# Kernel optimization log

Hardware: AMD Instinct MI355X
Metric: run time of the kernel (lower is better)

## Reference

```python
import jax, jax.numpy as jnp
import numpy as np

N_NODES = 50000
N_RAND_EDGES = 1_600_000
IN_FEATS = 512
HIDDEN = 256
NUM_CLASSES = 64


def setup_inputs() -> dict:
    key = jax.random.key(0)
    ks = jax.random.split(key, 6)
    src = jax.random.randint(ks[0], (N_RAND_EDGES,), 0, N_NODES, dtype=jnp.int32)
    dst = jax.random.randint(ks[1], (N_RAND_EDGES,), 0, N_NODES, dtype=jnp.int32)
    # dgl.add_self_loop(g): append (i, i) for every node
    loop = jnp.arange(N_NODES, dtype=jnp.int32)
    src = jnp.concatenate([src, loop])
    dst = jnp.concatenate([dst, loop])
    features = jax.random.normal(ks[2], (N_NODES, IN_FEATS), dtype=jnp.float32)
    W_conv = jax.random.normal(ks[3], (IN_FEATS, HIDDEN), dtype=jnp.float32) * (1.0 / np.sqrt(IN_FEATS))
    b_conv = jnp.zeros((HIDDEN,), dtype=jnp.float32)
    W2 = jax.random.normal(ks[4], (HIDDEN, NUM_CLASSES), dtype=jnp.float32) * (1.0 / np.sqrt(HIDDEN))
    b2 = jnp.zeros((NUM_CLASSES,), dtype=jnp.float32)
    return {"features": features, "W_conv": W_conv, "b_conv": b_conv,
            "W2": W2, "b2": b2, "src": src, "dst": dst}


def reference(features, W_conv, b_conv, W2, b2, src, dst):
    N = features.shape[0]
    ones = jnp.ones(src.shape[0], dtype=features.dtype)
    # symmetric ('both') normalization as in DGL GraphConv; self-loops guarantee deg >= 1
    deg_out = jax.ops.segment_sum(ones, src, num_segments=N)
    deg_in = jax.ops.segment_sum(ones, dst, num_segments=N)
    norm_src = jax.lax.rsqrt(deg_out)[:, None]  # [N, 1]
    norm_dst = jax.lax.rsqrt(deg_in)[:, None]
    # in_feats > hidden -> DGL multiplies by the weight before aggregating
    h = (features @ W_conv) * norm_src            # [N, H]
    agg = jax.ops.segment_sum(h[src], dst, num_segments=N)  # sparse SpMM: gather + scatter-add
    x = jax.nn.relu(agg * norm_dst + b_conv)      # [N, H]
    # dropout: identity in eval mode (deterministic reference)
    logits = x @ W2 + b2                          # [N, C]
    return jax.nn.log_softmax(logits, axis=1)
```

## Files before the change

kernel.cpp:

```cpp
#include <hip/hip_runtime.h>

typedef unsigned char u8;
typedef unsigned short u16;
typedef unsigned int u32;
typedef __attribute__((ext_vector_type(4))) float f32x4;
typedef __attribute__((ext_vector_type(8))) short s16x8;
typedef __attribute__((ext_vector_type(4))) unsigned short u16x4;
typedef __attribute__((ext_vector_type(8))) unsigned short u16x8;

#define IN_FEATS 512
#define HIDDEN   256
#define NCLS     64
#define NB       256
#define HBINS    25000
#define EPT      7

#define H8_CLIP  2.5f
#define H8_INV   (127.0f / H8_CLIP)
#define H8_SCALE (H8_CLIP / 127.0f)

static __device__ inline u16 f2bf(float f) {
    unsigned int u = __builtin_bit_cast(unsigned int, f);
    unsigned int r = (u + 0x7FFFu + ((u >> 16) & 1u)) >> 16;
    return (u16)r;
}


__launch_bounds__(1024)
__global__ void khist(const int* __restrict__ src, const int* __restrict__ dst,
                      u16* __restrict__ P,
                      const float* __restrict__ W, u16* __restrict__ Wt,
                      const float* __restrict__ W2, u16* __restrict__ W2t,
                      signed char* __restrict__ h8, int E, int N) {
    __shared__ u32 pk[25000];
    const int b = blockIdx.x;
    const int t = threadIdx.x;
    const int lo = (int)((long)b * E / NB);
    const int hi = (int)((long)(b + 1) * E / NB);

    {
        int g = b * 1024 + t;
        if (g < IN_FEATS * HIDDEN) {
            int k = g >> 8, n = g & 255;
            Wt[n * IN_FEATS + k] = f2bf(W[g]);
        } else if (g < IN_FEATS * HIDDEN + HIDDEN * NCLS) {
            int ii = g - IN_FEATS * HIDDEN;
            int k = ii >> 6, n = ii & 63;
            W2t[n * HIDDEN + k] = f2bf(W2[ii]);
        } else if (g < IN_FEATS * HIDDEN + HIDDEN * NCLS + 64) {
            ((int*)(h8 + (size_t)N * HIDDEN))[g - IN_FEATS * HIDDEN - HIDDEN * NCLS] = 0;
        }
    }

    int se[EPT], de[EPT];
#pragma unroll
    for (int p = 0; p < EPT; p++) {
        int e = lo + t + p * 1024;
        se[p] = 0; de[p] = 0;
        if (e < hi) { se[p] = src[e]; de[p] = dst[e]; }
    }

#pragma unroll 1
    for (int half = 0; half < 2; half++) {
        const int base = half * HBINS;
        __syncthreads();
        for (int j = t; j < 25000; j += 1024) pk[j] = 0;
        __syncthreads();
#pragma unroll
        for (int p = 0; p < EPT; p++) {
            int e = lo + t + p * 1024;
            if (e < hi) {
                unsigned rs = (unsigned)(se[p] - base), rd = (unsigned)(de[p] - base);
                if (rs < (unsigned)HBINS) atomicAdd(&pk[rs >> 1], 1u << ((rs & 1) << 4));
                if (rd < (unsigned)HBINS) atomicAdd(&pk[12500 + (rd >> 1)], 1u << ((rd & 1) << 4));
            }
        }
        for (int e = lo + t + EPT * 1024; e < hi; e += 1024) {
            int s = src[e], d = dst[e];
            unsigned rs = (unsigned)(s - base), rd = (unsigned)(d - base);
            if (rs < (unsigned)HBINS) atomicAdd(&pk[rs >> 1], 1u << ((rs & 1) << 4));
            if (rd < (unsigned)HBINS) atomicAdd(&pk[12500 + (rd >> 1)], 1u << ((rd & 1) << 4));
        }
        __syncthreads();
        for (int j = t; j < HBINS; j += 1024) {
            u32 o  = (pk[j >> 1] >> ((j & 1) << 4)) & 0xffffu;
            u32 in = (pk[12500 + (j >> 1)] >> ((j & 1) << 4)) & 0xffffu;
            P[(size_t)b * 50000 + base + j] = (u16)((o & 0xffu) | ((in & 0xffu) << 8));
        }
    }
}

__launch_bounds__(256)
__global__ void kredscan(u16* __restrict__ P, int* __restrict__ rowptr,
                         int* __restrict__ bsum, float* __restrict__ ns,
                         float* __restrict__ nd, int N) {
    __shared__ int wsum[4];
    const int b = blockIdx.x, t = threadIdx.x;
    const int lane = t & 63, wave = t >> 6;
    const int j = b * 256 + t;
    u32 si = 0;
    if (j < N) {
        u32 so = 0;
#pragma unroll 8
        for (int bb = 0; bb < NB; bb++) {
            u32 v = P[(size_t)bb * 50000 + j];
            P[(size_t)bb * 50000 + j] = (u16)si;
            so += v & 0xffu;
            si += v >> 8;
        }
        ns[j] = rsqrtf((float)so);
        nd[j] = rsqrtf((float)si);
    }
    int v = (j < N) ? (int)si : 0;
    int s = v;
#pragma unroll
    for (int off = 1; off < 64; off <<= 1) {
        int u = __shfl_up(s, off);
        if (lane >= off) s += u;
    }
    if (lane == 63) wsum[wave] = s;
    __syncthreads();
    int woff = 0;
#pragma unroll
    for (int w = 0; w < 4; w++) woff += (w < wave) ? wsum[w] : 0;
    if (j < N) rowptr[j] = woff + s - v;
    if (t == 255) bsum[b] = woff + s;
}

__launch_bounds__(256)
__global__ void kscanB(int* __restrict__ rowptr, const int* __restrict__ bsum,
                       int N, int nblk, int E) {
    __shared__ int wsum[4];
    const int b = blockIdx.x, t = threadIdx.x;
    const int lane = t & 63, wave = t >> 6;
    int v = (t < b && t < nblk) ? bsum[t] : 0;
#pragma unroll
    for (int off = 32; off; off >>= 1) v += __shfl_xor(v, off);
    if (lane == 0) wsum[wave] = v;
    __syncthreads();
    int offsum = wsum[0] + wsum[1] + wsum[2] + wsum[3];
    int j = b * 256 + t;
    if (j < N) rowptr[j] += offsum;
    if (b == 0 && t == 0) rowptr[N] = E;
}

__launch_bounds__(1024)
__global__ void kscat(const int* __restrict__ src, const int* __restrict__ dst,
                      const int* __restrict__ rowptr, const u16* __restrict__ P,
                      int* __restrict__ csc, int E, int N) {
    __shared__ int cur[HBINS];
    const int b = blockIdx.x;
    const int t = threadIdx.x;
    const int lo = (int)((long)b * E / NB);
    const int hi = (int)((long)(b + 1) * E / NB);

    int se[EPT], de[EPT];
#pragma unroll
    for (int p = 0; p < EPT; p++) {
        int e = lo + t + p * 1024;
        se[p] = 0; de[p] = 0;
        if (e < hi) { se[p] = src[e]; de[p] = dst[e]; }
    }

#pragma unroll 1
    for (int half = 0; half < 2; half++) {
        const int base = half * HBINS;
        __syncthreads();
        for (int j = t; j < HBINS; j += 1024) {
            int node = base + j;
            cur[j] = (node < N) ? rowptr[node] + (int)P[(size_t)b * 50000 + node] : 0;
        }
        __syncthreads();
#pragma unroll
        for (int p = 0; p < EPT; p++) {
            int e = lo + t + p * 1024;
            if (e < hi) {
                unsigned rd = (unsigned)(de[p] - base);
                if (rd < (unsigned)HBINS) {
                    int pos = atomicAdd(&cur[rd], 1);
                    csc[pos] = se[p] << 8;
                }
            }
        }
        for (int e = lo + t + EPT * 1024; e < hi; e += 1024) {
            int d = dst[e];
            unsigned rd = (unsigned)(d - base);
            if (rd < (unsigned)HBINS) {
                int pos = atomicAdd(&cur[rd], 1);
                csc[pos] = src[e] << 8;
            }
        }
    }
}


static __device__ inline s16x8 ld_frag(const u16* p) {
    u16x4 lo = *(const u16x4*)p;
    u16x4 hi = *(const u16x4*)(p + 4);
    s16x8 r;
    r[0] = (short)lo.x; r[1] = (short)lo.y; r[2] = (short)lo.z; r[3] = (short)lo.w;
    r[4] = (short)hi.x; r[5] = (short)hi.y; r[6] = (short)hi.z; r[7] = (short)hi.w;
    return r;
}

__launch_bounds__(512)
__global__ void k_gemm1(const float* __restrict__ feat, const u16* __restrict__ Wt,
                        const float* __restrict__ norm_src, signed char* __restrict__ h8, int N) {
    __shared__ __align__(16) u16 At[128][40];
    __shared__ __align__(16) u16 Bt[256][40];
    const int t = threadIdx.x;
    const int lane = t & 63;
    const int wave = t >> 6;
    const int wm = wave & 1;
    const int wn = wave >> 1;
    const int m0 = blockIdx.x * 128;
    const int l15 = lane & 15;
    const int l4 = lane >> 4;

    const int r0a = t >> 3, qa = t & 7;
    const int r1a = (t + 512) >> 3;
    const int gr0 = m0 + r0a, gr1 = m0 + r1a;

    float4 pa0, pa1;
    auto LOADA = [&](int kk) {
        pa0 = (gr0 < N) ? *(const float4*)&feat[(size_t)gr0 * IN_FEATS + kk + qa * 4]
                        : make_float4(0.f, 0.f, 0.f, 0.f);
        pa1 = (gr1 < N) ? *(const float4*)&feat[(size_t)gr1 * IN_FEATS + kk + qa * 4]
                        : make_float4(0.f, 0.f, 0.f, 0.f);
    };

    f32x4 acc[4][4] = {};
    LOADA(0);

    for (int kk = 0; kk < IN_FEATS; kk += 32) {
        __syncthreads();
        {
            u16x4 p;
            p.x = f2bf(pa0.x); p.y = f2bf(pa0.y); p.z = f2bf(pa0.z); p.w = f2bf(pa0.w);
            *(u16x4*)&At[r0a][qa * 4] = p;
            p.x = f2bf(pa1.x); p.y = f2bf(pa1.y); p.z = f2bf(pa1.z); p.w = f2bf(pa1.w);
            *(u16x4*)&At[r1a][qa * 4] = p;
        }
#pragma unroll
        for (int rnd = 0; rnd < 2; rnd++) {
            int slot = t + rnd * 512;
            int r = slot >> 2, q = slot & 3;
            u16x4 w0 = *(const u16x4*)&Wt[(size_t)r * IN_FEATS + kk + q * 8];
            u16x4 w1 = *(const u16x4*)&Wt[(size_t)r * IN_FEATS + kk + q * 8 + 4];
            *(u16x4*)&Bt[r][q * 8] = w0;
            *(u16x4*)&Bt[r][q * 8 + 4] = w1;
        }
        if (kk + 32 < IN_FEATS) LOADA(kk + 32);
        __syncthreads();

        s16x8 a[4], b[4];
#pragma unroll
        for (int mi = 0; mi < 4; mi++) a[mi] = ld_frag(&At[wm * 64 + mi * 16 + l15][l4 * 8]);
#pragma unroll
        for (int ni = 0; ni < 4; ni++) b[ni] = ld_frag(&Bt[wn * 64 + ni * 16 + l15][l4 * 8]);
#pragma unroll
        for (int mi = 0; mi < 4; mi++)
#pragma unroll
            for (int ni = 0; ni < 4; ni++)
                acc[mi][ni] = __builtin_amdgcn_mfma_f32_16x16x32_bf16(a[mi], b[ni], acc[mi][ni], 0, 0, 0);
    }

#pragma unroll
    for (int mi = 0; mi < 4; mi++) {
#pragma unroll
        for (int q = 0; q < 4; q++) {
            int row = m0 + wm * 64 + mi * 16 + l4 * 4 + q;
            if (row < N) {
                float nsv = norm_src[row] * H8_INV;
#pragma unroll
                for (int ni = 0; ni < 4; ni++) {
                    int col = wn * 64 + ni * 16 + l15;
                    int v = (int)rintf(acc[mi][ni][q] * nsv);
                    v = max(-127, min(127, v));
                    h8[(size_t)row * HIDDEN + col] = (signed char)v;
                }
            }
        }
    }
}

__launch_bounds__(256)
__global__ void k_spmm(const signed char* __restrict__ h8, const int* __restrict__ rowptr,
                       const int* __restrict__ csc, const float* __restrict__ nd,
                       const float* __restrict__ bconv, u16* __restrict__ x, int N) {
    const int t = threadIdx.x;
    const int lane = t & 63;
    const int half = lane >> 5;
    const int hl = lane & 31;
    const int ZOFF = N * HIDDEN;
    const int gw = (blockIdx.x * blockDim.x + t) >> 6;
    const int nw = (gridDim.x * blockDim.x) >> 6;
    const int npair = (N + 1) >> 1;

    for (int pair = gw; pair < npair; pair += nw) {
        int node = pair * 2 + half;
        bool valid = node < N;
        int start = 0, deg = 0;
        if (valid) { start = rowptr[node]; deg = rowptr[node + 1] - start; }
        int maxdeg = max(deg, __shfl_xor(deg, 32));
        int a0 = 0, a1 = 0, a2 = 0, a3 = 0, a4 = 0, a5 = 0, a6 = 0, a7 = 0;

        for (int base = 0; base < maxdeg; base += 32) {
            int ev = ZOFF;
            if (base + hl < deg) ev = csc[start + base + hl];
            int cntmax = min(32, maxdeg - base);
            int i = 0;
            for (; i + 4 <= cntmax; i += 4) {
                int sb = (half << 5) + i;
                int o0 = __shfl(ev, sb);
                int o1 = __shfl(ev, sb + 1);
                int o2 = __shfl(ev, sb + 2);
                int o3 = __shfl(ev, sb + 3);
                int2 w0 = *(const int2*)&h8[o0 + hl * 8];
                int2 w1 = *(const int2*)&h8[o1 + hl * 8];
                int2 w2 = *(const int2*)&h8[o2 + hl * 8];
                int2 w3 = *(const int2*)&h8[o3 + hl * 8];
                a0 += ((w0.x << 24) >> 24) + ((w1.x << 24) >> 24) + ((w2.x << 24) >> 24) + ((w3.x << 24) >> 24);
                a1 += ((w0.x << 16) >> 24) + ((w1.x << 16) >> 24) + ((w2.x << 16) >> 24) + ((w3.x << 16) >> 24);
                a2 += ((w0.x << 8) >> 24) + ((w1.x << 8) >> 24) + ((w2.x << 8) >> 24) + ((w3.x << 8) >> 24);
                a3 += (w0.x >> 24) + (w1.x >> 24) + (w2.x >> 24) + (w3.x >> 24);
                a4 += ((w0.y << 24) >> 24) + ((w1.y << 24) >> 24) + ((w2.y << 24) >> 24) + ((w3.y << 24) >> 24);
                a5 += ((w0.y << 16) >> 24) + ((w1.y << 16) >> 24) + ((w2.y << 16) >> 24) + ((w3.y << 16) >> 24);
                a6 += ((w0.y << 8) >> 24) + ((w1.y << 8) >> 24) + ((w2.y << 8) >> 24) + ((w3.y << 8) >> 24);
                a7 += (w0.y >> 24) + (w1.y >> 24) + (w2.y >> 24) + (w3.y >> 24);
            }
            for (; i < cntmax; i++) {
                int o = __shfl(ev, (half << 5) + i);
                int2 w = *(const int2*)&h8[o + hl * 8];
                a0 += (w.x << 24) >> 24;
                a1 += (w.x << 16) >> 24;
                a2 += (w.x << 8) >> 24;
                a3 += w.x >> 24;
                a4 += (w.y << 24) >> 24;
                a5 += (w.y << 16) >> 24;
                a6 += (w.y << 8) >> 24;
                a7 += w.y >> 24;
            }
        }

        if (valid) {
            float scnd = nd[node] * H8_SCALE;
            float4 ba = *(const float4*)&bconv[hl * 8];
            float4 bb = *(const float4*)&bconv[hl * 8 + 4];
            u16x8 o;
            o[0] = f2bf(fmaxf((float)a0 * scnd + ba.x, 0.f));
            o[1] = f2bf(fmaxf((float)a1 * scnd + ba.y, 0.f));
            o[2] = f2bf(fmaxf((float)a2 * scnd + ba.z, 0.f));
            o[3] = f2bf(fmaxf((float)a3 * scnd + ba.w, 0.f));
            o[4] = f2bf(fmaxf((float)a4 * scnd + bb.x, 0.f));
            o[5] = f2bf(fmaxf((float)a5 * scnd + bb.y, 0.f));
            o[6] = f2bf(fmaxf((float)a6 * scnd + bb.z, 0.f));
            o[7] = f2bf(fmaxf((float)a7 * scnd + bb.w, 0.f));
            *(u16x8*)&x[(size_t)node * HIDDEN + hl * 8] = o;
        }
    }
}

__launch_bounds__(256)
__global__ void k_gemm2(const u16* __restrict__ x, const u16* __restrict__ W2t,
                        const float* __restrict__ b2, float* __restrict__ out, int N) {
    __shared__ __align__(16) u16 Bs[NCLS][HIDDEN + 8];
    const int t = threadIdx.x;
    for (int i = t; i < NCLS * HIDDEN / 8; i += 256) {
        int idx = i * 8;
        int n = idx >> 8, k = idx & 255;
        *(u16x8*)&Bs[n][k] = *(const u16x8*)&W2t[n * HIDDEN + k];
    }
    __syncthreads();

    const int lane = t & 63;
    const int wave = t >> 6;
    const int l15 = lane & 15;
    const int l4 = lane >> 4;
    const int r0 = blockIdx.x * 128 + wave * 32;

    float bb[4];
#pragma unroll
    for (int ni = 0; ni < 4; ni++) bb[ni] = b2[ni * 16 + l15];

    f32x4 acc[2][4] = {};
#pragma unroll
    for (int kk = 0; kk < HIDDEN; kk += 32) {
        s16x8 b[4];
#pragma unroll
        for (int ni = 0; ni < 4; ni++) b[ni] = ld_frag(&Bs[ni * 16 + l15][kk + l4 * 8]);
#pragma unroll
        for (int mi = 0; mi < 2; mi++) {
            int row = r0 + mi * 16 + l15;
            s16x8 a = {};
            if (row < N) a = ld_frag(&x[(size_t)row * HIDDEN + kk + l4 * 8]);
#pragma unroll
            for (int ni = 0; ni < 4; ni++)
                acc[mi][ni] = __builtin_amdgcn_mfma_f32_16x16x32_bf16(a, b[ni], acc[mi][ni], 0, 0, 0);
        }
    }

#pragma unroll
    for (int mi = 0; mi < 2; mi++) {
#pragma unroll
        for (int q = 0; q < 4; q++) {
            int row = r0 + mi * 16 + l4 * 4 + q;
            float v0 = acc[mi][0][q] + bb[0];
            float v1 = acc[mi][1][q] + bb[1];
            float v2 = acc[mi][2][q] + bb[2];
            float v3 = acc[mi][3][q] + bb[3];
            float m = fmaxf(fmaxf(v0, v1), fmaxf(v2, v3));
#pragma unroll
            for (int off = 1; off < 16; off <<= 1) m = fmaxf(m, __shfl_xor(m, off));
            float s = __expf(v0 - m) + __expf(v1 - m) + __expf(v2 - m) + __expf(v3 - m);
#pragma unroll
            for (int off = 1; off < 16; off <<= 1) s += __shfl_xor(s, off);
            float lg = m + __logf(s);
            if (row < N) {
                out[(size_t)row * NCLS + 0 * 16 + l15] = v0 - lg;
                out[(size_t)row * NCLS + 1 * 16 + l15] = v1 - lg;
                out[(size_t)row * NCLS + 2 * 16 + l15] = v2 - lg;
                out[(size_t)row * NCLS + 3 * 16 + l15] = v3 - lg;
            }
        }
    }
}


extern "C" void kernel_launch(void* const* d_in, const int* in_sizes, int n_in,
                              void* d_out, int out_size, void* d_ws, size_t ws_size,
                              hipStream_t stream) {
    const float* feat = (const float*)d_in[0];
    const float* Wc   = (const float*)d_in[1];
    const float* bc   = (const float*)d_in[2];
    const float* W2   = (const float*)d_in[3];
    const float* b2   = (const float*)d_in[4];
    const int*   src  = (const int*)d_in[5];
    const int*   dst  = (const int*)d_in[6];
    const int N = in_sizes[0] / IN_FEATS;
    const int E = in_sizes[5];
    float* out = (float*)d_out;

    char* ws = (char*)d_ws;
    size_t off = 0;
    auto alloc = [&](size_t b) {
        char* p = ws + off;
        off = (off + b + 255) & ~(size_t)255;
        return p;
    };
    signed char* h8 = (signed char*)alloc((size_t)(N + 1) * HIDDEN);
    u16* x      = (u16*)alloc((size_t)N * HIDDEN * 2);
    u16* Wt     = (u16*)alloc((size_t)IN_FEATS * HIDDEN * 2);
    u16* W2t    = (u16*)alloc((size_t)HIDDEN * NCLS * 2);
    int* rowptr = (int*)alloc((size_t)(N + 1) * 4);
    int* bsum   = (int*)alloc((size_t)256 * 4);
    float* ns   = (float*)alloc((size_t)N * 4);
    float* nd   = (float*)alloc((size_t)N * 4);
    int* csc    = (int*)alloc((size_t)E * 4);
    u16* P      = (u16*)alloc((size_t)NB * 50000 * 2);

    const int nblk = (N + 255) / 256;

    khist<<<dim3(NB), dim3(1024), 0, stream>>>(src, dst, P, Wc, Wt, W2, W2t, h8, E, N);
    kredscan<<<dim3(nblk), dim3(256), 0, stream>>>(P, rowptr, bsum, ns, nd, N);
    kscanB<<<dim3(nblk), dim3(256), 0, stream>>>(rowptr, bsum, N, nblk, E);
    kscat<<<dim3(NB), dim3(1024), 0, stream>>>(src, dst, rowptr, P, csc, E, N);
    k_gemm1<<<dim3((N + 127) / 128), dim3(512), 0, stream>>>(feat, Wt, ns, h8, N);
    k_spmm<<<dim3(2048), dim3(256), 0, stream>>>(h8, rowptr, csc, nd, bc, x, N);
    k_gemm2<<<dim3((N + 127) / 128), dim3(256), 0, stream>>>(x, W2t, b2, out, N);
}
```

Baseline: 160.4 us.

## Build degree histogram and CSC scatter in a single pass with packed LDS counters

The degree histogram now packs four 8-bit counters per 32-bit LDS word for both out- and in-degree. That lets all 50000 nodes fit in shared memory at once, so the two-half pass over the edges and its register prefetch arrays go away. The CSC scatter also runs in one pass: it uses 16-bit packed per-block counters and reads rowptr and the per-block prefix offset per edge from global memory, instead of preloading a cursor table per half. This removes a full re-scan of the edges and the bulk cursor initialisation, at the cost of two random global loads per edge and an 8-bit per-block count limit.

```diff
diff --git a/kernel.cpp b/kernel.cpp
--- a/kernel.cpp
+++ b/kernel.cpp
@@ -12,9 +12,6 @@
 #define HIDDEN   256
 #define NCLS     64
 #define NB       256
-#define HBINS    25000
-#define EPT      7
-
 #define H8_CLIP  2.5f
 #define H8_INV   (127.0f / H8_CLIP)
 #define H8_SCALE (H8_CLIP / 127.0f)
@@ -32,7 +29,8 @@
                       const float* __restrict__ W, u16* __restrict__ Wt,
                       const float* __restrict__ W2, u16* __restrict__ W2t,
                       signed char* __restrict__ h8, int E, int N) {
-    __shared__ u32 pk[25000];
+    __shared__ u32 ob[12500];
+    __shared__ u32 ib[12500];
     const int b = blockIdx.x;
     const int t = threadIdx.x;
     const int lo = (int)((long)b * E / NB);
@@ -52,41 +50,20 @@
         }
     }
 
-    int se[EPT], de[EPT];
-#pragma unroll
-    for (int p = 0; p < EPT; p++) {
-        int e = lo + t + p * 1024;
-        se[p] = 0; de[p] = 0;
-        if (e < hi) { se[p] = src[e]; de[p] = dst[e]; }
-    }
-
-#pragma unroll 1
-    for (int half = 0; half < 2; half++) {
-        const int base = half * HBINS;
-        __syncthreads();
-        for (int j = t; j < 25000; j += 1024) pk[j] = 0;
-        __syncthreads();
-#pragma unroll
-        for (int p = 0; p < EPT; p++) {
-            int e = lo + t + p * 1024;
-            if (e < hi) {
-                unsigned rs = (unsigned)(se[p] - base), rd = (unsigned)(de[p] - base);
-                if (rs < (unsigned)HBINS) atomicAdd(&pk[rs >> 1], 1u << ((rs & 1) << 4));
-                if (rd < (unsigned)HBINS) atomicAdd(&pk[12500 + (rd >> 1)], 1u << ((rd & 1) << 4));
-            }
-        }
-        for (int e = lo + t + EPT * 1024; e < hi; e += 1024) {
-            int s = src[e], d = dst[e];
-            unsigned rs = (unsigned)(s - base), rd = (unsigned)(d - base);
-            if (rs < (unsigned)HBINS) atomicAdd(&pk[rs >> 1], 1u << ((rs & 1) << 4));
-            if (rd < (unsigned)HBINS) atomicAdd(&pk[12500 + (rd >> 1)], 1u << ((rd & 1) << 4));
-        }
-        __syncthreads();
-        for (int j = t; j < HBINS; j += 1024) {
-            u32 o  = (pk[j >> 1] >> ((j & 1) << 4)) & 0xffffu;
-            u32 in = (pk[12500 + (j >> 1)] >> ((j & 1) << 4)) & 0xffffu;
-            P[(size_t)b * 50000 + base + j] = (u16)((o & 0xffu) | ((in & 0xffu) << 8));
-        }
+    for (int j = t; j < 12500; j += 1024) { ob[j] = 0; ib[j] = 0; }
+    __syncthreads();
+
+    for (int e = lo + t; e < hi; e += 1024) {
+        int s = src[e], d = dst[e];
+        atomicAdd(&ob[s >> 2], 1u << ((s & 3) << 3));
+        atomicAdd(&ib[d >> 2], 1u << ((d & 3) << 3));
+    }
+    __syncthreads();
+
+    for (int j = t; j < 50000; j += 1024) {
+        u32 o  = (ob[j >> 2] >> ((j & 3) << 3)) & 0xffu;
+        u32 in = (ib[j >> 2] >> ((j & 3) << 3)) & 0xffu;
+        P[(size_t)b * 50000 + j] = (u16)(o | (in << 8));
     }
 }
 
@@ -148,48 +125,22 @@
 __global__ void kscat(const int* __restrict__ src, const int* __restrict__ dst,
                       const int* __restrict__ rowptr, const u16* __restrict__ P,
                       int* __restrict__ csc, int E, int N) {
-    __shared__ int cur[HBINS];
+    __shared__ u32 cnt[25000];
     const int b = blockIdx.x;
     const int t = threadIdx.x;
     const int lo = (int)((long)b * E / NB);
     const int hi = (int)((long)(b + 1) * E / NB);
 
-    int se[EPT], de[EPT];
-#pragma unroll
-    for (int p = 0; p < EPT; p++) {
-        int e = lo + t + p * 1024;
-        se[p] = 0; de[p] = 0;
-        if (e < hi) { se[p] = src[e]; de[p] = dst[e]; }
-    }
-
-#pragma unroll 1
-    for (int half = 0; half < 2; half++) {
-        const int base = half * HBINS;
-        __syncthreads();
-        for (int j = t; j < HBINS; j += 1024) {
-            int node = base + j;
-            cur[j] = (node < N) ? rowptr[node] + (int)P[(size_t)b * 50000 + node] : 0;
-        }
-        __syncthreads();
-#pragma unroll
-        for (int p = 0; p < EPT; p++) {
-            int e = lo + t + p * 1024;
-            if (e < hi) {
-                unsigned rd = (unsigned)(de[p] - base);
-                if (rd < (unsigned)HBINS) {
-                    int pos = atomicAdd(&cur[rd], 1);
-                    csc[pos] = se[p] << 8;
-                }
-            }
-        }
-        for (int e = lo + t + EPT * 1024; e < hi; e += 1024) {
-            int d = dst[e];
-            unsigned rd = (unsigned)(d - base);
-            if (rd < (unsigned)HBINS) {
-                int pos = atomicAdd(&cur[rd], 1);
-                csc[pos] = src[e] << 8;
-            }
-        }
+    for (int j = t; j < 25000; j += 1024) cnt[j] = 0;
+    __syncthreads();
+
+    for (int e = lo + t; e < hi; e += 1024) {
+        int s = src[e], d = dst[e];
+        int sh = (d & 1) << 4;
+        u32 old = atomicAdd(&cnt[d >> 1], 1u << sh);
+        int local = (int)((old >> sh) & 0xffffu);
+        int pos = rowptr[d] + (int)P[(size_t)b * 50000 + d] + local;
+        csc[pos] = s << 8;
     }
 }
 
```

Result: slower. 164.4 us (+2.5%).
